# Kernel tuning notes

Measured on AMD Instinct MI355X. Metric: run time of the kernel, lower is better.

Reference implementation:

```python
import jax, jax.numpy as jnp
import numpy as np

EMB_TABLE = 80000  # full shared embedding rows
N_ITEMS = 50000    # target item count (item_num + 1)
E = 600000         # edges
D = 128            # embedding_size
L = 3              # num_gcn_layers


def gcn_conv(x, W, b, src, dst, norm, n):
    # PyG GCNConv: x' = lin(x); out[i] = sum_{(j->i)} norm_ji * x'[j] + bias
    msgs = (x @ W)[src] * norm[:, None]          # [E+n, D]
    out = jax.ops.segment_sum(msgs, dst, num_segments=n)
    return out + b


def setup_inputs() -> dict:
    key = jax.random.key(0)
    k0, k1, k2 = jax.random.split(key, 3)
    item_emb = jax.random.normal(k0, (EMB_TABLE, D), dtype=jnp.float32) * 0.02
    weights = jax.random.normal(k1, (L, D, D), dtype=jnp.float32) * (1.0 / np.sqrt(D))
    biases = jnp.zeros((L, D), dtype=jnp.float32)
    edge_index = jax.random.randint(k2, (2, E), 0, N_ITEMS, dtype=jnp.int64)
    return {"item_emb": item_emb, "weights": weights, "biases": biases,
            "edge_index": edge_index, "item_nums": N_ITEMS}


def reference(item_emb, weights, biases, edge_index, item_nums):
    n = item_nums
    x0 = item_emb[-n:]  # embeds[0] = item_emb[-item_nums:]
    loops = jnp.arange(n, dtype=edge_index.dtype)
    src = jnp.concatenate([edge_index[0], loops])  # add self-loops (GCNConv default)
    dst = jnp.concatenate([edge_index[1], loops])
    # symmetric normalization: deg computed on target side with self-loops
    deg = jax.ops.segment_sum(jnp.ones_like(src, dtype=x0.dtype), dst, num_segments=n)
    dinv = jnp.where(deg > 0, jax.lax.rsqrt(jnp.maximum(deg, 1e-12)), 0.0)
    norm = dinv[src] * dinv[dst]                   # [E+n]
    embeds = [x0]
    for l in range(weights.shape[0]):
        embeds.append(gcn_conv(embeds[-1], weights[l], biases[l], src, dst, norm, n))
    total = embeds[0]
    for e in embeds[1:]:
        total = total + e
    return (total, *embeds)
```

## Files before the change

kernel.cpp:

```cpp
#include <hip/hip_runtime.h>
#include <stdint.h>

#define D 128

typedef unsigned int u32;
typedef unsigned short u16;
typedef __attribute__((ext_vector_type(8))) short short8;
typedef __attribute__((ext_vector_type(4))) float f32x4;

static __device__ __forceinline__ float bf2f(u16 h) {
    return __uint_as_float(((u32)h) << 16);
}
static __device__ __forceinline__ u16 f2bf(float f) {
    u32 u = __float_as_uint(f);
    u32 r = (u + 0x7fffu + ((u >> 16) & 1u)) >> 16;
    return (u16)r;
}
static __device__ __forceinline__ int clampi(int v, int n) {
    if (v < 0) v = 0;
    if (v >= n) v = n - 1;
    return v;
}
static __device__ __forceinline__ int bf_plausible(u16 h) {
    u32 ex = (h >> 7) & 0xFF;
    return (h == 0 || (ex >= 0x60 && ex <= 0x8F)) ? 1 : 0;
}

__global__ __launch_bounds__(256) void k_a(int* __restrict__ hist, int* __restrict__ csr_pos,
                                           u32* __restrict__ state, int n, int nbk,
                                           const u16* __restrict__ emb16,
                                           const u32* __restrict__ ei,
                                           const u16* __restrict__ w16,
                                           int* __restrict__ flags, u16* __restrict__ WB,
                                           int off_elems, int nD4,
                                           float* __restrict__ out_x0) {
    int bid = blockIdx.x, t = threadIdx.x;
    __shared__ int ps[256];
    if (bid < nbk) {
        int i = bid * 256 + t;
        if (i < n) {
            hist[i] = 0;
            csr_pos[i] = 0;
        }
        if (i < nbk) state[i] = 0;
        if (bid == 0 && t < 64) {
            int se = 0, sw = 0, zz = 0;
#pragma unroll
            for (int q = 0; q < 4; q++) {
                int k = t * 4 + q;
                se += bf_plausible(emb16[2 * k]);
                sw += bf_plausible(w16[2 * k]);
                if (ei[2 * k + 1] == 0) zz++;
            }
#pragma unroll
            for (int o = 32; o; o >>= 1) {
                se += __shfl_down(se, o);
                sw += __shfl_down(sw, o);
                zz += __shfl_down(zz, o);
            }
            if (t == 0) {
                flags[0] = (se >= 200) ? 1 : 0;
                flags[2] = (sw >= 200) ? 1 : 0;
                flags[1] = (zz >= 200) ? 1 : 0;
            }
        }
    } else if (bid < nbk + 192) {
        ps[t] = bf_plausible(w16[2 * t]);
        __syncthreads();
        for (int o = 128; o; o >>= 1) {
            if (t < o) ps[t] += ps[t + o];
            __syncthreads();
        }
        int wf = (ps[0] >= 200);
        int idx = (bid - nbk) * 256 + t;
        int e = idx & 7;
        int l = (idx >> 3) & 63;
        int ks = (idx >> 9) & 3;
        int c = (idx >> 11) & 7;
        int layer = idx >> 14;
        int k = ks * 32 + ((l >> 4) << 3) + e;
        int j = (c << 4) + (l & 15);
        size_t src = (size_t)layer * D * D + (size_t)k * D + j;
        float wv = wf ? bf2f(w16[src]) : ((const float*)w16)[src];
        u16 hb = f2bf(wv);
        u16 lb = f2bf(wv - bf2f(hb));
        size_t o = (size_t)layer * 32768 + (size_t)((c * 4 + ks) * 64 + l) * 8 + e;
        WB[o] = hb;
        WB[o + 16384] = lb;
    } else {
        ps[t] = bf_plausible(emb16[2 * t]);
        __syncthreads();
        for (int o = 128; o; o >>= 1) {
            if (t < o) ps[t] += ps[t + o];
            __syncthreads();
        }
        int ef = (ps[0] >= 200);
        int i = (bid - nbk - 192) * 256 + t;
        if (i < nD4) {
            float4 v;
            if (ef) {
                ushort4 h = ((const ushort4*)(emb16 + off_elems))[i];
                v = make_float4(bf2f(h.x), bf2f(h.y), bf2f(h.z), bf2f(h.w));
            } else {
                v = ((const float4*)((const float*)emb16 + off_elems))[i];
            }
            ((float4*)out_x0)[i] = v;
        }
    }
}

__global__ __launch_bounds__(256) void k_b(const u32* __restrict__ ei, int E, int n,
                                           const int* __restrict__ flags,
                                           int* __restrict__ hist,
                                           const float* __restrict__ A0,
                                           const u16* __restrict__ WB,
                                           u32* __restrict__ Y0, int eb) {
    int bid = blockIdx.x, tid = threadIdx.x;
    if (bid < eb) {
        int e = bid * 256 + tid;
        if (e >= E) return;
        int d;
        if (flags[1]) d = ((const int2*)ei)[(size_t)E + e].x;
        else          d = (int)ei[(size_t)E + e];
        atomicAdd(&hist[clampi(d, n)], 1);
    } else {
        int bg = bid - eb;
        int w = tid >> 6, l = tid & 63;
        int row0 = bg * 64 + w * 16;
        int ar = row0 + (l & 15);
        if (ar >= n) ar = 0;
        const float* Ab = A0 + (size_t)ar * D + ((l >> 4) << 3);
        f32x4 acc[8] = {};
        const short8* bp = (const short8*)WB;
#pragma unroll
        for (int ks = 0; ks < 4; ks++) {
            f32x4 a0 = *(const f32x4*)(Ab + ks * 32);
            f32x4 a1 = *(const f32x4*)(Ab + ks * 32 + 4);
            float av[8] = {a0.x, a0.y, a0.z, a0.w, a1.x, a1.y, a1.z, a1.w};
            short8 ah, al;
#pragma unroll
            for (int e2 = 0; e2 < 8; e2++) {
                u16 h = f2bf(av[e2]);
                ah[e2] = (short)h;
                al[e2] = (short)f2bf(av[e2] - bf2f(h));
            }
#pragma unroll
            for (int c = 0; c < 8; c++) {
                short8 bh = bp[(c * 4 + ks) * 64 + l];
                short8 bl = bp[2048 + (c * 4 + ks) * 64 + l];
                acc[c] = __builtin_amdgcn_mfma_f32_16x16x32_bf16(al, bh, acc[c], 0, 0, 0);
                acc[c] = __builtin_amdgcn_mfma_f32_16x16x32_bf16(ah, bl, acc[c], 0, 0, 0);
                acc[c] = __builtin_amdgcn_mfma_f32_16x16x32_bf16(ah, bh, acc[c], 0, 0, 0);
            }
        }
        int rbase = row0 + ((l >> 4) << 2);
        int col = l & 15;
#pragma unroll
        for (int r = 0; r < 4; r++) {
            int gr = rbase + r;
            if (gr < n) {
#pragma unroll
                for (int c = 0; c < 4; c++) {
                    u32 pack = (u32)f2bf(acc[c][r]) | ((u32)f2bf(acc[c + 4][r]) << 16);
                    Y0[(size_t)gr * 64 + c * 16 + col] = pack;
                }
            }
        }
    }
}

__global__ __launch_bounds__(256) void k_scan(const int* __restrict__ hist, int n,
                                              u32* __restrict__ state,
                                              int* __restrict__ csr_off,
                                              float* __restrict__ dinv) {
    __shared__ int s[256];
    __shared__ int excl_sh;
    int t = threadIdx.x, b = blockIdx.x;
    int i = b * 256 + t;
    int h = (i < n) ? hist[i] : 0;
    s[t] = h;
    __syncthreads();
    for (int d2 = 1; d2 < 256; d2 <<= 1) {
        int add = (t >= d2) ? s[t - d2] : 0;
        __syncthreads();
        s[t] += add;
        __syncthreads();
    }
    int agg = s[255];
    if (t == 0) {
        if (b == 0) {
            __hip_atomic_store(&state[0], (2u << 30) | (u32)agg, __ATOMIC_RELEASE,
                               __HIP_MEMORY_SCOPE_AGENT);
            excl_sh = 0;
        } else {
            __hip_atomic_store(&state[b], (1u << 30) | (u32)agg, __ATOMIC_RELEASE,
                               __HIP_MEMORY_SCOPE_AGENT);
            int run = 0;
            int idx = b - 1;
            while (true) {
                u32 v = __hip_atomic_load(&state[idx], __ATOMIC_ACQUIRE,
                                          __HIP_MEMORY_SCOPE_AGENT);
                u32 f = v >> 30;
                if (f == 0) {
                    __builtin_amdgcn_s_sleep(1);
                    continue;
                }
                run += (int)(v & 0x3fffffffu);
                if (f == 2u) break;
                idx--;
            }
            __hip_atomic_store(&state[b], (2u << 30) | (u32)(run + agg), __ATOMIC_RELEASE,
                               __HIP_MEMORY_SCOPE_AGENT);
            excl_sh = run;
        }
    }
    __syncthreads();
    int excl = excl_sh;
    if (i < n) {
        csr_off[i] = excl + s[t] - h;
        dinv[i] = rsqrtf((float)(h + 1));
    }
}

__global__ void k_sx(const u32* __restrict__ ei, int E, int n,
                     const int* __restrict__ flags,
                     const int* __restrict__ csr_off, int* __restrict__ csr_pos,
                     const float* __restrict__ dinv, int2* __restrict__ csr_pair) {
    int e = blockIdx.x * 256 + threadIdx.x;
    if (e >= E) return;
    int s, d;
    if (flags[1]) {
        s = ((const int2*)ei)[e].x;
        d = ((const int2*)ei)[(size_t)E + e].x;
    } else {
        s = (int)ei[e];
        d = (int)ei[(size_t)E + e];
    }
    s = clampi(s, n);
    d = clampi(d, n);
    int p = csr_off[d] + atomicAdd(&csr_pos[d], 1);
    if (p >= E) p = E - 1;
    csr_pair[p] = make_int2(s, __float_as_int(dinv[s] * dinv[d]));
}

__global__ __launch_bounds__(256, 4) void k_ag(const u32* __restrict__ Yin,
                                               const int* __restrict__ csr_off,
                                               const int* __restrict__ cnt,
                                               const int2* __restrict__ csr_pair,
                                               const float* __restrict__ dinv,
                                               const void* __restrict__ bias_base, int layer,
                                               const int* __restrict__ flags, int n, int nD,
                                               float* __restrict__ out_x,
                                               float* __restrict__ out_tot,
                                               const float* __restrict__ out_base,
                                               const u16* __restrict__ WB, int gemm_layer,
                                               u32* __restrict__ Yout) {
    __shared__ float xt[64 * 132];
    int tid = threadIdx.x;
    int w = tid >> 6, t = tid & 63;
    int g = t >> 4, p = t & 15;
    int i0 = blockIdx.x * 64;

#define ACC4(V, W)                                                       \
    do {                                                                 \
        lo0 += __uint_as_float((V).x << 16) * (W);                       \
        hi0 += __uint_as_float((V).x & 0xffff0000u) * (W);               \
        lo1 += __uint_as_float((V).y << 16) * (W);                       \
        hi1 += __uint_as_float((V).y & 0xffff0000u) * (W);               \
        lo2 += __uint_as_float((V).z << 16) * (W);                       \
        hi2 += __uint_as_float((V).z & 0xffff0000u) * (W);               \
        lo3 += __uint_as_float((V).w << 16) * (W);                       \
        hi3 += __uint_as_float((V).w & 0xffff0000u) * (W);               \
    } while (0)

    for (int q = 0; q < 16; q++) {
        int i = i0 + (w << 4) + q;
        if (i >= n) break;

        float lo0 = 0.f, lo1 = 0.f, lo2 = 0.f, lo3 = 0.f;
        float hi0 = 0.f, hi1 = 0.f, hi2 = 0.f, hi3 = 0.f;

        float di = dinv[i];
        {
            uint4 vs = *(const uint4*)(Yin + (size_t)i * 64 + p * 4);
            float ws = (g == 0) ? di * di : 0.0f;
            ACC4(vs, ws);
        }
        int start = csr_off[i];
        int c = cnt[i];
        for (int base = 0; base < c; base += 64) {
            int m = c - base;
            if (m > 64) m = 64;
            int2 pr = (t < m) ? csr_pair[start + base + t] : make_int2(0, 0);
            int s0 = __shfl(pr.x, g);
            float w0 = __uint_as_float((u32)__shfl(pr.y, g));
            uint4 v0 = *(const uint4*)(Yin + (size_t)s0 * 64 + p * 4);
            for (int j = 4; j < m; j += 4) {
                int s1 = __shfl(pr.x, j + g);
                float w1 = __uint_as_float((u32)__shfl(pr.y, j + g));
                uint4 v1 = *(const uint4*)(Yin + (size_t)s1 * 64 + p * 4);
                ACC4(v0, w0);
                v0 = v1;
                w0 = w1;
            }
            ACC4(v0, w0);
        }
#pragma unroll
        for (int mask = 16; mask <= 32; mask <<= 1) {
            lo0 += __shfl_xor(lo0, mask);
            lo1 += __shfl_xor(lo1, mask);
            lo2 += __shfl_xor(lo2, mask);
            lo3 += __shfl_xor(lo3, mask);
            hi0 += __shfl_xor(hi0, mask);
            hi1 += __shfl_xor(hi1, mask);
            hi2 += __shfl_xor(hi2, mask);
            hi3 += __shfl_xor(hi3, mask);
        }
        if (g < 2) {
            float r0 = g ? hi0 : lo0;
            float r1 = g ? hi1 : lo1;
            float r2 = g ? hi2 : lo2;
            float r3 = g ? hi3 : lo3;
            int off = g * 64 + 4 * p;
            float b0, b1, b2, b3;
            if (flags[0]) {
                const u16* bb = (const u16*)bias_base + layer * D + off;
                ushort4 h = *(const ushort4*)bb;
                b0 = bf2f(h.x); b1 = bf2f(h.y); b2 = bf2f(h.z); b3 = bf2f(h.w);
            } else {
                const float* bb = (const float*)bias_base + layer * D + off;
                float4 f = *(const float4*)bb;
                b0 = f.x; b1 = f.y; b2 = f.z; b3 = f.w;
            }
            float4 xv = make_float4(r0 + b0, r1 + b1, r2 + b2, r3 + b3);
            *(float4*)&xt[((w << 4) + q) * 132 + off] = xv;
            size_t gbase = (size_t)i * D + off;
            *(float4*)&out_x[gbase] = xv;
            if (out_tot) {
                float4 s0 = *(const float4*)&out_base[(size_t)1 * nD + gbase];
                float4 s1 = *(const float4*)&out_base[(size_t)2 * nD + gbase];
                float4 s2 = *(const float4*)&out_base[(size_t)3 * nD + gbase];
                *(float4*)&out_tot[gbase] =
                    make_float4(s0.x + s1.x + s2.x + xv.x, s0.y + s1.y + s2.y + xv.y,
                                s0.z + s1.z + s2.z + xv.z, s0.w + s1.w + s2.w + xv.w);
            }
        }
    }
#undef ACC4

    if (gemm_layer >= 0) {
        __syncthreads();
        int row0 = i0 + (w << 4);
        int rl = (w << 4) + (t & 15);
        const float* Ab = &xt[rl * 132 + ((t >> 4) << 3)];
        f32x4 acc[8] = {};
        const short8* bp = (const short8*)(WB + (size_t)gemm_layer * 32768);
#pragma unroll
        for (int ks = 0; ks < 4; ks++) {
            f32x4 a0 = *(const f32x4*)(Ab + ks * 32);
            f32x4 a1 = *(const f32x4*)(Ab + ks * 32 + 4);
            float av[8] = {a0.x, a0.y, a0.z, a0.w, a1.x, a1.y, a1.z, a1.w};
            short8 ah, al;
#pragma unroll
            for (int e2 = 0; e2 < 8; e2++) {
                u16 h = f2bf(av[e2]);
                ah[e2] = (short)h;
                al[e2] = (short)f2bf(av[e2] - bf2f(h));
            }
#pragma unroll
            for (int c = 0; c < 8; c++) {
                short8 bh = bp[(c * 4 + ks) * 64 + t];
                short8 bl = bp[2048 + (c * 4 + ks) * 64 + t];
                acc[c] = __builtin_amdgcn_mfma_f32_16x16x32_bf16(al, bh, acc[c], 0, 0, 0);
                acc[c] = __builtin_amdgcn_mfma_f32_16x16x32_bf16(ah, bl, acc[c], 0, 0, 0);
                acc[c] = __builtin_amdgcn_mfma_f32_16x16x32_bf16(ah, bh, acc[c], 0, 0, 0);
            }
        }
        int rbase = row0 + ((t >> 4) << 2);
        int col = t & 15;
#pragma unroll
        for (int r = 0; r < 4; r++) {
            int gr = rbase + r;
            if (gr < n) {
#pragma unroll
                for (int c = 0; c < 4; c++) {
                    u32 pack = (u32)f2bf(acc[c][r]) | ((u32)f2bf(acc[c + 4][r]) << 16);
                    Yout[(size_t)gr * 64 + c * 16 + col] = pack;
                }
            }
        }
    }
}

extern "C" void kernel_launch(void* const* d_in, const int* in_sizes, int n_in,
                              void* d_out, int out_size, void* d_ws, size_t ws_size,
                              hipStream_t stream) {
    float* out = (float*)d_out;

    const int n = out_size / (5 * D);

    int i_emb = -1, i_ei = -1, i_w = -1, i_b = -1;
    {
        int order[8];
        int m = n_in > 8 ? 8 : n_in;
        for (int i = 0; i < m; i++) order[i] = i;
        for (int a = 0; a < m; a++)
            for (int b2 = a + 1; b2 < m; b2++)
                if (in_sizes[order[b2]] > in_sizes[order[a]]) {
                    int tmp = order[a]; order[a] = order[b2]; order[b2] = tmp;
                }
        i_emb = order[0];
        i_ei  = (m > 1) ? order[1] : 0;
        for (int i = 0; i < m; i++) {
            if (in_sizes[i] == 3 * D * D && i_w < 0) i_w = i;
            if (in_sizes[i] == 3 * D && i_b < 0) i_b = i;
        }
        if (i_w < 0) i_w = (m > 2) ? order[2] : 0;
        if (i_b < 0) i_b = (m > 3) ? order[3] : 0;
    }
    const void* emb  = d_in[i_emb];
    const void* wts  = d_in[i_w];
    const void* bias = d_in[i_b];
    const u32*  ei   = (const u32*)d_in[i_ei];

    const int E = in_sizes[i_ei] / 2;
    const int rows = in_sizes[i_emb] / D;
    const int off_elems = (rows - n) * D;

    char* p = (char*)d_ws;
    auto take = [&](size_t bytes) {
        char* r = p;
        p += (bytes + 255) & ~(size_t)255;
        return r;
    };
    const int nD = n * D;
    const int nb = (n + 255) / 256;
    const int eb = (E + 255) / 256;
    const int x0b = (nD / 4 + 255) / 256;
    const int gb = (n + 63) / 64;

    int*   flags    = (int*)  take(3 * 4);
    int*   hist     = (int*)  take((size_t)n * 4);
    int*   csr_pos  = (int*)  take((size_t)n * 4);
    int*   csr_off  = (int*)  take((size_t)n * 4);
    u32*   state    = (u32*)  take((size_t)nb * 4);
    float* dinv     = (float*)take((size_t)n * 4);
    int2*  csr_pair = (int2*) take((size_t)E * 8);
    u32*   yA       = (u32*)  take((size_t)n * 64 * 4);
    u32*   yB       = (u32*)  take((size_t)n * 64 * 4);
    u16*   wb       = (u16*)  take((size_t)3 * 32768 * 2);

    float* x0 = out + (size_t)nD;

    k_a<<<nb + 192 + x0b, 256, 0, stream>>>(hist, csr_pos, state, n, nb, (const u16*)emb,
                                            ei, (const u16*)wts, flags, wb, off_elems,
                                            nD / 4, x0);
    k_b<<<eb + gb, 256, 0, stream>>>(ei, E, n, flags, hist, x0, wb, yA, eb);
    k_scan<<<nb, 256, 0, stream>>>(hist, n, state, csr_off, dinv);
    k_sx<<<eb, 256, 0, stream>>>(ei, E, n, flags, csr_off, csr_pos, dinv, csr_pair);

    k_ag<<<gb, 256, 0, stream>>>(yA, csr_off, hist, csr_pair, dinv, bias, 0, flags, n, nD,
                                 out + (size_t)2 * nD, (float*)nullptr, out, wb, 1, yB);
    k_ag<<<gb, 256, 0, stream>>>(yB, csr_off, hist, csr_pair, dinv, bias, 1, flags, n, nD,
                                 out + (size_t)3 * nD, (float*)nullptr, out, wb, 2, yA);
    k_ag<<<gb, 256, 0, stream>>>(yA, csr_off, hist, csr_pair, dinv, bias, 2, flags, n, nD,
                                 out + (size_t)4 * nD, out, out, wb, -1, (u32*)nullptr);
}
```

Measured before the change: 431.4 us.

## Split fused aggregate+GEMM into separate kernels and regroup the setup launches

Splits the fused per-layer aggregation+GEMM kernel into a wave-per-node aggregation kernel and a standalone GEMM kernel that stages the split bf16 weights in LDS. The launch grouping also changes: the weight split moves alongside the histogram pass, and the first GEMM is merged with the prefix scan. The aim is more parallelism and occupancy in the gather phase and fewer global weight loads in the GEMM. In exchange it adds launches and round-trips each layer's output through global memory before the next GEMM, and the layer-0 GEMM now shares a launch with a spin-waiting scan.

New measurement: 378.5 us. 1.14x faster.

```diff
diff --git a/kernel.cpp b/kernel.cpp
--- a/kernel.cpp
+++ b/kernel.cpp
@@ -26,16 +26,15 @@
     return (h == 0 || (ex >= 0x60 && ex <= 0x8F)) ? 1 : 0;
 }
 
-__global__ __launch_bounds__(256) void k_a(int* __restrict__ hist, int* __restrict__ csr_pos,
-                                           u32* __restrict__ state, int n, int nbk,
-                                           const u16* __restrict__ emb16,
-                                           const u32* __restrict__ ei,
-                                           const u16* __restrict__ w16,
-                                           int* __restrict__ flags, u16* __restrict__ WB,
-                                           int off_elems, int nD4,
-                                           float* __restrict__ out_x0) {
+__global__ __launch_bounds__(256) void k_init(int* __restrict__ hist, int* __restrict__ csr_pos,
+                                              u32* __restrict__ state, int n, int nbk,
+                                              const u16* __restrict__ emb16,
+                                              const u32* __restrict__ ei,
+                                              const u16* __restrict__ w16,
+                                              int* __restrict__ flags,
+                                              int off_elems, int nD4,
+                                              float* __restrict__ out_x0) {
     int bid = blockIdx.x, t = threadIdx.x;
-    __shared__ int ps[256];
     if (bid < nbk) {
         int i = bid * 256 + t;
         if (i < n) {
@@ -64,15 +63,42 @@
                 flags[1] = (zz >= 200) ? 1 : 0;
             }
         }
-    } else if (bid < nbk + 192) {
-        ps[t] = bf_plausible(w16[2 * t]);
+    } else {
+        __shared__ int ps[256];
+        ps[t] = bf_plausible(emb16[2 * t]);
         __syncthreads();
         for (int o = 128; o; o >>= 1) {
             if (t < o) ps[t] += ps[t + o];
             __syncthreads();
         }
-        int wf = (ps[0] >= 200);
-        int idx = (bid - nbk) * 256 + t;
+        int ef = (ps[0] >= 200);
+        int i = (bid - nbk) * 256 + t;
+        if (i < nD4) {
+            float4 v;
+            if (ef) {
+                ushort4 h = ((const ushort4*)(emb16 + off_elems))[i];
+                v = make_float4(bf2f(h.x), bf2f(h.y), bf2f(h.z), bf2f(h.w));
+            } else {
+                v = ((const float4*)((const float*)emb16 + off_elems))[i];
+            }
+            ((float4*)out_x0)[i] = v;
+        }
+    }
+}
+
+__global__ void k_hw(const u32* __restrict__ ei, int E, int n,
+                     const int* __restrict__ flags, int* __restrict__ hist,
+                     const void* __restrict__ Wbase, u16* __restrict__ WB, int eb) {
+    int bid = blockIdx.x;
+    if (bid < eb) {
+        int e = bid * 256 + threadIdx.x;
+        if (e >= E) return;
+        int d;
+        if (flags[1]) d = ((const int2*)ei)[(size_t)E + e].x;
+        else          d = (int)ei[(size_t)E + e];
+        atomicAdd(&hist[clampi(d, n)], 1);
+    } else {
+        int idx = (bid - eb) * 256 + threadIdx.x;
         int e = idx & 7;
         int l = (idx >> 3) & 63;
         int ks = (idx >> 9) & 3;
@@ -81,57 +107,89 @@
         int k = ks * 32 + ((l >> 4) << 3) + e;
         int j = (c << 4) + (l & 15);
         size_t src = (size_t)layer * D * D + (size_t)k * D + j;
-        float wv = wf ? bf2f(w16[src]) : ((const float*)w16)[src];
-        u16 hb = f2bf(wv);
-        u16 lb = f2bf(wv - bf2f(hb));
+        float w = flags[2] ? bf2f(((const u16*)Wbase)[src]) : ((const float*)Wbase)[src];
+        u16 hb = f2bf(w);
+        u16 lb = f2bf(w - bf2f(hb));
         size_t o = (size_t)layer * 32768 + (size_t)((c * 4 + ks) * 64 + l) * 8 + e;
         WB[o] = hb;
         WB[o + 16384] = lb;
+    }
+}
+
+__global__ __launch_bounds__(256) void k_sg(const int* __restrict__ hist, int n,
+                                            u32* __restrict__ state,
+                                            int* __restrict__ csr_off,
+                                            float* __restrict__ dinv,
+                                            const float* __restrict__ A0,
+                                            const u16* __restrict__ WB,
+                                            u32* __restrict__ Y0, int nbk) {
+    __shared__ f32x4 ldsv[4096];
+    __shared__ int excl_sh;
+    int t = threadIdx.x, b = blockIdx.x;
+    if (b < nbk) {
+        int* s = (int*)ldsv;
+        int i = b * 256 + t;
+        int h = (i < n) ? hist[i] : 0;
+        s[t] = h;
+        __syncthreads();
+        for (int d2 = 1; d2 < 256; d2 <<= 1) {
+            int add = (t >= d2) ? s[t - d2] : 0;
+            __syncthreads();
+            s[t] += add;
+            __syncthreads();
+        }
+        int agg = s[255];
+        if (t == 0) {
+            if (b == 0) {
+                __hip_atomic_store(&state[0], (2u << 30) | (u32)agg, __ATOMIC_RELEASE,
+                                   __HIP_MEMORY_SCOPE_AGENT);
+                excl_sh = 0;
+            } else {
+                __hip_atomic_store(&state[b], (1u << 30) | (u32)agg, __ATOMIC_RELEASE,
+                                   __HIP_MEMORY_SCOPE_AGENT);
+                int run = 0;
+                int idx = b - 1;
+                while (true) {
+                    u32 v = __hip_atomic_load(&state[idx], __ATOMIC_ACQUIRE,
+                                              __HIP_MEMORY_SCOPE_AGENT);
+                    u32 f = v >> 30;
+                    if (f == 0) {
+                        __builtin_amdgcn_s_sleep(1);
+                        continue;
+                    }
+                    run += (int)(v & 0x3fffffffu);
+                    if (f == 2u) break;
+                    idx--;
+                }
+                __hip_atomic_store(&state[b], (2u << 30) | (u32)(run + agg), __ATOMIC_RELEASE,
+                                   __HIP_MEMORY_SCOPE_AGENT);
+                excl_sh = run;
+            }
+        }
+        __syncthreads();
+        int excl = excl_sh;
+        if (i < n) {
+            csr_off[i] = excl + s[t] - h;
+            dinv[i] = rsqrtf((float)(h + 1));
+        }
     } else {
-        ps[t] = bf_plausible(emb16[2 * t]);
+        int tid = t;
+        {
+            const f32x4* src = (const f32x4*)WB;
+#pragma unroll
+            for (int i = 0; i < 16; i++) ldsv[tid + 256 * i] = src[tid + 256 * i];
+        }
         __syncthreads();
-        for (int o = 128; o; o >>= 1) {
-            if (t < o) ps[t] += ps[t + o];
-            __syncthreads();
-        }
-        int ef = (ps[0] >= 200);
-        int i = (bid - nbk - 192) * 256 + t;
-        if (i < nD4) {
-            float4 v;
-            if (ef) {
-                ushort4 h = ((const ushort4*)(emb16 + off_elems))[i];
-                v = make_float4(bf2f(h.x), bf2f(h.y), bf2f(h.z), bf2f(h.w));
-            } else {
-                v = ((const float4*)((const float*)emb16 + off_elems))[i];
-            }
-            ((float4*)out_x0)[i] = v;
-        }
-    }
-}
-
-__global__ __launch_bounds__(256) void k_b(const u32* __restrict__ ei, int E, int n,
-                                           const int* __restrict__ flags,
-                                           int* __restrict__ hist,
-                                           const float* __restrict__ A0,
-                                           const u16* __restrict__ WB,
-                                           u32* __restrict__ Y0, int eb) {
-    int bid = blockIdx.x, tid = threadIdx.x;
-    if (bid < eb) {
-        int e = bid * 256 + tid;
-        if (e >= E) return;
-        int d;
-        if (flags[1]) d = ((const int2*)ei)[(size_t)E + e].x;
-        else          d = (int)ei[(size_t)E + e];
-        atomicAdd(&hist[clampi(d, n)], 1);
-    } else {
-        int bg = bid - eb;
+
         int w = tid >> 6, l = tid & 63;
-        int row0 = bg * 64 + w * 16;
+        int row0 = (b - nbk) * 64 + w * 16;
         int ar = row0 + (l & 15);
         if (ar >= n) ar = 0;
         const float* Ab = A0 + (size_t)ar * D + ((l >> 4) << 3);
+
         f32x4 acc[8] = {};
-        const short8* bp = (const short8*)WB;
+        const short8* bp = (const short8*)ldsv;
+
 #pragma unroll
         for (int ks = 0; ks < 4; ks++) {
             f32x4 a0 = *(const f32x4*)(Ab + ks * 32);
@@ -139,10 +197,10 @@
             float av[8] = {a0.x, a0.y, a0.z, a0.w, a1.x, a1.y, a1.z, a1.w};
             short8 ah, al;
 #pragma unroll
-            for (int e2 = 0; e2 < 8; e2++) {
-                u16 h = f2bf(av[e2]);
-                ah[e2] = (short)h;
-                al[e2] = (short)f2bf(av[e2] - bf2f(h));
+            for (int e = 0; e < 8; e++) {
+                u16 h = f2bf(av[e]);
+                ah[e] = (short)h;
+                al[e] = (short)f2bf(av[e] - bf2f(h));
             }
 #pragma unroll
             for (int c = 0; c < 8; c++) {
@@ -153,6 +211,7 @@
                 acc[c] = __builtin_amdgcn_mfma_f32_16x16x32_bf16(ah, bh, acc[c], 0, 0, 0);
             }
         }
+
         int rbase = row0 + ((l >> 4) << 2);
         int col = l & 15;
 #pragma unroll
@@ -166,59 +225,6 @@
                 }
             }
         }
-    }
-}
-
-__global__ __launch_bounds__(256) void k_scan(const int* __restrict__ hist, int n,
-                                              u32* __restrict__ state,
-                                              int* __restrict__ csr_off,
-                                              float* __restrict__ dinv) {
-    __shared__ int s[256];
-    __shared__ int excl_sh;
-    int t = threadIdx.x, b = blockIdx.x;
-    int i = b * 256 + t;
-    int h = (i < n) ? hist[i] : 0;
-    s[t] = h;
-    __syncthreads();
-    for (int d2 = 1; d2 < 256; d2 <<= 1) {
-        int add = (t >= d2) ? s[t - d2] : 0;
-        __syncthreads();
-        s[t] += add;
-        __syncthreads();
-    }
-    int agg = s[255];
-    if (t == 0) {
-        if (b == 0) {
-            __hip_atomic_store(&state[0], (2u << 30) | (u32)agg, __ATOMIC_RELEASE,
-                               __HIP_MEMORY_SCOPE_AGENT);
-            excl_sh = 0;
-        } else {
-            __hip_atomic_store(&state[b], (1u << 30) | (u32)agg, __ATOMIC_RELEASE,
-                               __HIP_MEMORY_SCOPE_AGENT);
-            int run = 0;
-            int idx = b - 1;
-            while (true) {
-                u32 v = __hip_atomic_load(&state[idx], __ATOMIC_ACQUIRE,
-                                          __HIP_MEMORY_SCOPE_AGENT);
-                u32 f = v >> 30;
-                if (f == 0) {
-                    __builtin_amdgcn_s_sleep(1);
-                    continue;
-                }
-                run += (int)(v & 0x3fffffffu);
-                if (f == 2u) break;
-                idx--;
-            }
-            __hip_atomic_store(&state[b], (2u << 30) | (u32)(run + agg), __ATOMIC_RELEASE,
-                               __HIP_MEMORY_SCOPE_AGENT);
-            excl_sh = run;
-        }
-    }
-    __syncthreads();
-    int excl = excl_sh;
-    if (i < n) {
-        csr_off[i] = excl + s[t] - h;
-        dinv[i] = rsqrtf((float)(h + 1));
     }
 }
 
@@ -243,23 +249,81 @@
     csr_pair[p] = make_int2(s, __float_as_int(dinv[s] * dinv[d]));
 }
 
-__global__ __launch_bounds__(256, 4) void k_ag(const u32* __restrict__ Yin,
-                                               const int* __restrict__ csr_off,
-                                               const int* __restrict__ cnt,
-                                               const int2* __restrict__ csr_pair,
-                                               const float* __restrict__ dinv,
-                                               const void* __restrict__ bias_base, int layer,
-                                               const int* __restrict__ flags, int n, int nD,
-                                               float* __restrict__ out_x,
-                                               float* __restrict__ out_tot,
-                                               const float* __restrict__ out_base,
-                                               const u16* __restrict__ WB, int gemm_layer,
-                                               u32* __restrict__ Yout) {
-    __shared__ float xt[64 * 132];
+__global__ __launch_bounds__(256) void k_gemm(const float* __restrict__ A,
+                                              const u16* __restrict__ WB, int layer,
+                                              int n, u32* __restrict__ Y) {
+    __shared__ f32x4 ldsv[4096];
     int tid = threadIdx.x;
-    int w = tid >> 6, t = tid & 63;
+    {
+        const f32x4* src = (const f32x4*)(WB + (size_t)layer * 32768);
+#pragma unroll
+        for (int i = 0; i < 16; i++) ldsv[tid + 256 * i] = src[tid + 256 * i];
+    }
+    __syncthreads();
+
+    int w = tid >> 6, l = tid & 63;
+    int row0 = blockIdx.x * 64 + w * 16;
+    int ar = row0 + (l & 15);
+    if (ar >= n) ar = 0;
+    const float* Ab = A + (size_t)ar * D + ((l >> 4) << 3);
+
+    f32x4 acc[8] = {};
+    const short8* bp = (const short8*)ldsv;
+
+#pragma unroll
+    for (int ks = 0; ks < 4; ks++) {
+        f32x4 a0 = *(const f32x4*)(Ab + ks * 32);
+        f32x4 a1 = *(const f32x4*)(Ab + ks * 32 + 4);
+        float av[8] = {a0.x, a0.y, a0.z, a0.w, a1.x, a1.y, a1.z, a1.w};
+        short8 ah, al;
+#pragma unroll
+        for (int e = 0; e < 8; e++) {
+            u16 h = f2bf(av[e]);
+            ah[e] = (short)h;
+            al[e] = (short)f2bf(av[e] - bf2f(h));
+        }
+#pragma unroll
+        for (int c = 0; c < 8; c++) {
+            short8 bh = bp[(c * 4 + ks) * 64 + l];
+            short8 bl = bp[2048 + (c * 4 + ks) * 64 + l];
+            acc[c] = __builtin_amdgcn_mfma_f32_16x16x32_bf16(al, bh, acc[c], 0, 0, 0);
+            acc[c] = __builtin_amdgcn_mfma_f32_16x16x32_bf16(ah, bl, acc[c], 0, 0, 0);
+            acc[c] = __builtin_amdgcn_mfma_f32_16x16x32_bf16(ah, bh, acc[c], 0, 0, 0);
+        }
+    }
+
+    int rbase = row0 + ((l >> 4) << 2);
+    int col = l & 15;
+#pragma unroll
+    for (int r = 0; r < 4; r++) {
+        int gr = rbase + r;
+        if (gr < n) {
+#pragma unroll
+            for (int c = 0; c < 4; c++) {
+                u32 pack = (u32)f2bf(acc[c][r]) | ((u32)f2bf(acc[c + 4][r]) << 16);
+                Y[(size_t)gr * 64 + c * 16 + col] = pack;
+            }
+        }
+    }
+}
+
+__global__ __launch_bounds__(256) void k_agg(const u32* __restrict__ Y,
+                                             const int* __restrict__ csr_off,
+                                             const int* __restrict__ cnt,
+                                             const int2* __restrict__ csr_pair,
+                                             const float* __restrict__ dinv,
+                                             const void* __restrict__ bias_base, int layer,
+                                             const int* __restrict__ flags, int n, int nD,
+                                             const float* __restrict__ out_base,
+                                             float* __restrict__ out_x,
+                                             float* __restrict__ out_tot) {
+    int i = blockIdx.x * 4 + (threadIdx.x >> 6);
+    if (i >= n) return;
+    int t = threadIdx.x & 63;
     int g = t >> 4, p = t & 15;
-    int i0 = blockIdx.x * 64;
+
+    float lo0 = 0.f, lo1 = 0.f, lo2 = 0.f, lo3 = 0.f;
+    float hi0 = 0.f, hi1 = 0.f, hi2 = 0.f, hi3 = 0.f;
 
 #define ACC4(V, W)                                                       \
     do {                                                                 \
@@ -273,121 +337,74 @@
         hi3 += __uint_as_float((V).w & 0xffff0000u) * (W);               \
     } while (0)
 
-    for (int q = 0; q < 16; q++) {
-        int i = i0 + (w << 4) + q;
-        if (i >= n) break;
-
-        float lo0 = 0.f, lo1 = 0.f, lo2 = 0.f, lo3 = 0.f;
-        float hi0 = 0.f, hi1 = 0.f, hi2 = 0.f, hi3 = 0.f;
-
-        float di = dinv[i];
-        {
-            uint4 vs = *(const uint4*)(Yin + (size_t)i * 64 + p * 4);
-            float ws = (g == 0) ? di * di : 0.0f;
-            ACC4(vs, ws);
-        }
-        int start = csr_off[i];
-        int c = cnt[i];
-        for (int base = 0; base < c; base += 64) {
-            int m = c - base;
-            if (m > 64) m = 64;
-            int2 pr = (t < m) ? csr_pair[start + base + t] : make_int2(0, 0);
-            int s0 = __shfl(pr.x, g);
-            float w0 = __uint_as_float((u32)__shfl(pr.y, g));
-            uint4 v0 = *(const uint4*)(Yin + (size_t)s0 * 64 + p * 4);
-            for (int j = 4; j < m; j += 4) {
-                int s1 = __shfl(pr.x, j + g);
-                float w1 = __uint_as_float((u32)__shfl(pr.y, j + g));
-                uint4 v1 = *(const uint4*)(Yin + (size_t)s1 * 64 + p * 4);
-                ACC4(v0, w0);
-                v0 = v1;
-                w0 = w1;
-            }
+    float di = dinv[i];
+    {
+        uint4 vs = *(const uint4*)(Y + (size_t)i * 64 + p * 4);
+        float ws = (g == 0) ? di * di : 0.0f;
+        ACC4(vs, ws);
+    }
+
+    int start = csr_off[i];
+    int c = cnt[i];
+
+    for (int base = 0; base < c; base += 64) {
+        int m = c - base;
+        if (m > 64) m = 64;
+        int2 pr = (t < m) ? csr_pair[start + base + t] : make_int2(0, 0);
+        int s0 = __shfl(pr.x, g);
+        float w0 = __uint_as_float((u32)__shfl(pr.y, g));
+        uint4 v0 = *(const uint4*)(Y + (size_t)s0 * 64 + p * 4);
+        for (int j = 4; j < m; j += 4) {
+            int s1 = __shfl(pr.x, j + g);
+            float w1 = __uint_as_float((u32)__shfl(pr.y, j + g));
+            uint4 v1 = *(const uint4*)(Y + (size_t)s1 * 64 + p * 4);
             ACC4(v0, w0);
-        }
-#pragma unroll
-        for (int mask = 16; mask <= 32; mask <<= 1) {
-            lo0 += __shfl_xor(lo0, mask);
-            lo1 += __shfl_xor(lo1, mask);
-            lo2 += __shfl_xor(lo2, mask);
-            lo3 += __shfl_xor(lo3, mask);
-            hi0 += __shfl_xor(hi0, mask);
-            hi1 += __shfl_xor(hi1, mask);
-            hi2 += __shfl_xor(hi2, mask);
-            hi3 += __shfl_xor(hi3, mask);
-        }
-        if (g < 2) {
-            float r0 = g ? hi0 : lo0;
-            float r1 = g ? hi1 : lo1;
-            float r2 = g ? hi2 : lo2;
-            float r3 = g ? hi3 : lo3;
-            int off = g * 64 + 4 * p;
-            float b0, b1, b2, b3;
-            if (flags[0]) {
-                const u16* bb = (const u16*)bias_base + layer * D + off;
-                ushort4 h = *(const ushort4*)bb;
-                b0 = bf2f(h.x); b1 = bf2f(h.y); b2 = bf2f(h.z); b3 = bf2f(h.w);
-            } else {
-                const float* bb = (const float*)bias_base + layer * D + off;
-                float4 f = *(const float4*)bb;
-                b0 = f.x; b1 = f.y; b2 = f.z; b3 = f.w;
-            }
-            float4 xv = make_float4(r0 + b0, r1 + b1, r2 + b2, r3 + b3);
-            *(float4*)&xt[((w << 4) + q) * 132 + off] = xv;
-            size_t gbase = (size_t)i * D + off;
-            *(float4*)&out_x[gbase] = xv;
-            if (out_tot) {
-                float4 s0 = *(const float4*)&out_base[(size_t)1 * nD + gbase];
-                float4 s1 = *(const float4*)&out_base[(size_t)2 * nD + gbase];
-                float4 s2 = *(const float4*)&out_base[(size_t)3 * nD + gbase];
-                *(float4*)&out_tot[gbase] =
-                    make_float4(s0.x + s1.x + s2.x + xv.x, s0.y + s1.y + s2.y + xv.y,
-                                s0.z + s1.z + s2.z + xv.z, s0.w + s1.w + s2.w + xv.w);
-            }
-        }
+            v0 = v1;
+            w0 = w1;
+        }
+        ACC4(v0, w0);
     }
 #undef ACC4
 
-    if (gemm_layer >= 0) {
-        __syncthreads();
-        int row0 = i0 + (w << 4);
-        int rl = (w << 4) + (t & 15);
-        const float* Ab = &xt[rl * 132 + ((t >> 4) << 3)];
-        f32x4 acc[8] = {};
-        const short8* bp = (const short8*)(WB + (size_t)gemm_layer * 32768);
-#pragma unroll
-        for (int ks = 0; ks < 4; ks++) {
-            f32x4 a0 = *(const f32x4*)(Ab + ks * 32);
-            f32x4 a1 = *(const f32x4*)(Ab + ks * 32 + 4);
-            float av[8] = {a0.x, a0.y, a0.z, a0.w, a1.x, a1.y, a1.z, a1.w};
-            short8 ah, al;
-#pragma unroll
-            for (int e2 = 0; e2 < 8; e2++) {
-                u16 h = f2bf(av[e2]);
-                ah[e2] = (short)h;
-                al[e2] = (short)f2bf(av[e2] - bf2f(h));
-            }
-#pragma unroll
-            for (int c = 0; c < 8; c++) {
-                short8 bh = bp[(c * 4 + ks) * 64 + t];
-                short8 bl = bp[2048 + (c * 4 + ks) * 64 + t];
-                acc[c] = __builtin_amdgcn_mfma_f32_16x16x32_bf16(al, bh, acc[c], 0, 0, 0);
-                acc[c] = __builtin_amdgcn_mfma_f32_16x16x32_bf16(ah, bl, acc[c], 0, 0, 0);
-                acc[c] = __builtin_amdgcn_mfma_f32_16x16x32_bf16(ah, bh, acc[c], 0, 0, 0);
-            }
-        }
-        int rbase = row0 + ((t >> 4) << 2);
-        int col = t & 15;
-#pragma unroll
-        for (int r = 0; r < 4; r++) {
-            int gr = rbase + r;
-            if (gr < n) {
-#pragma unroll
-                for (int c = 0; c < 4; c++) {
-                    u32 pack = (u32)f2bf(acc[c][r]) | ((u32)f2bf(acc[c + 4][r]) << 16);
-                    Yout[(size_t)gr * 64 + c * 16 + col] = pack;
-                }
-            }
+#pragma unroll
+    for (int mask = 16; mask <= 32; mask <<= 1) {
+        lo0 += __shfl_xor(lo0, mask);
+        lo1 += __shfl_xor(lo1, mask);
+        lo2 += __shfl_xor(lo2, mask);
+        lo3 += __shfl_xor(lo3, mask);
+        hi0 += __shfl_xor(hi0, mask);
+        hi1 += __shfl_xor(hi1, mask);
+        hi2 += __shfl_xor(hi2, mask);
+        hi3 += __shfl_xor(hi3, mask);
+    }
+
+    if (g < 2) {
+        float r0 = g ? hi0 : lo0;
+        float r1 = g ? hi1 : lo1;
+        float r2 = g ? hi2 : lo2;
+        float r3 = g ? hi3 : lo3;
+        int off = g * 64 + 4 * p;
+        float b0, b1, b2, b3;
+        if (flags[0]) {
+            const u16* bb = (const u16*)bias_base + layer * D + off;
+            ushort4 h = *(const ushort4*)bb;
+            b0 = bf2f(h.x); b1 = bf2f(h.y); b2 = bf2f(h.z); b3 = bf2f(h.w);
+        } else {
+            const float* bb = (const float*)bias_base + layer * D + off;
+            float4 f = *(const float4*)bb;
+            b0 = f.x; b1 = f.y; b2 = f.z; b3 = f.w;
+        }
+        float4 xv = make_float4(r0 + b0, r1 + b1, r2 + b2, r3 + b3);
+        size_t base = (size_t)i * D + off;
+        *(float4*)&out_x[base] = xv;
+
+        if (out_tot) {
+            float4 s0 = *(const float4*)&out_base[(size_t)1 * nD + base];
+            float4 s1 = *(const float4*)&out_base[(size_t)2 * nD + base];
+            float4 s2 = *(const float4*)&out_base[(size_t)3 * nD + base];
+            *(float4*)&out_tot[base] =
+                make_float4(s0.x + s1.x + s2.x + xv.x, s0.y + s1.y + s2.y + xv.y,
+                            s0.z + s1.z + s2.z + xv.z, s0.w + s1.w + s2.w + xv.w);
         }
     }
 }
@@ -438,6 +455,7 @@
     const int eb = (E + 255) / 256;
     const int x0b = (nD / 4 + 255) / 256;
     const int gb = (n + 63) / 64;
+    const int ab = (n + 3) / 4;
 
     int*   flags    = (int*)  take(3 * 4);
     int*   hist     = (int*)  take((size_t)n * 4);
@@ -446,23 +464,24 @@
     u32*   state    = (u32*)  take((size_t)nb * 4);
     float* dinv     = (float*)take((size_t)n * 4);
     int2*  csr_pair = (int2*) take((size_t)E * 8);
-    u32*   yA       = (u32*)  take((size_t)n * 64 * 4);
-    u32*   yB       = (u32*)  take((size_t)n * 64 * 4);
+    u32*   ybuf     = (u32*)  take((size_t)n * 64 * 4);
     u16*   wb       = (u16*)  take((size_t)3 * 32768 * 2);
 
     float* x0 = out + (size_t)nD;
 
-    k_a<<<nb + 192 + x0b, 256, 0, stream>>>(hist, csr_pos, state, n, nb, (const u16*)emb,
-                                            ei, (const u16*)wts, flags, wb, off_elems,
-                                            nD / 4, x0);
-    k_b<<<eb + gb, 256, 0, stream>>>(ei, E, n, flags, hist, x0, wb, yA, eb);
-    k_scan<<<nb, 256, 0, stream>>>(hist, n, state, csr_off, dinv);
+    k_init<<<nb + x0b, 256, 0, stream>>>(hist, csr_pos, state, n, nb, (const u16*)emb,
+                                         ei, (const u16*)wts, flags, off_elems, nD / 4, x0);
+    k_hw<<<eb + 192, 256, 0, stream>>>(ei, E, n, flags, hist, wts, wb, eb);
+    k_sg<<<nb + gb, 256, 0, stream>>>(hist, n, state, csr_off, dinv, x0, wb, ybuf, nb);
     k_sx<<<eb, 256, 0, stream>>>(ei, E, n, flags, csr_off, csr_pos, dinv, csr_pair);
 
-    k_ag<<<gb, 256, 0, stream>>>(yA, csr_off, hist, csr_pair, dinv, bias, 0, flags, n, nD,
-                                 out + (size_t)2 * nD, (float*)nullptr, out, wb, 1, yB);
-    k_ag<<<gb, 256, 0, stream>>>(yB, csr_off, hist, csr_pair, dinv, bias, 1, flags, n, nD,
-                                 out + (size_t)3 * nD, (float*)nullptr, out, wb, 2, yA);
-    k_ag<<<gb, 256, 0, stream>>>(yA, csr_off, hist, csr_pair, dinv, bias, 2, flags, n, nD,
-                                 out + (size_t)4 * nD, out, out, wb, -1, (u32*)nullptr);
-}
+    for (int l = 0; l < 3; l++) {
+        float* ox = out + (size_t)(2 + l) * nD;
+        k_agg<<<ab, 256, 0, stream>>>(ybuf, csr_off, hist, csr_pair, dinv, bias, l,
+                                      flags, n, nD, out, ox,
+                                      (l == 2) ? out : (float*)nullptr);
+        if (l < 2) {
+            k_gemm<<<gb, 256, 0, stream>>>(ox, wb, l + 1, n, ybuf);
+        }
+    }
+}
```
